# Optimization experiments

Measured on AMD Instinct MI355X. Metric: run time of the kernel, lower is better.

The kernel has to match this reference:

```python
import jax, jax.numpy as jnp
import numpy as np

D2, D1, T1, T2, D3, T3 = 120, 40, 10, 5, 3, 1


def _kaiming_uniform(key, shape):
    # torch kaiming_uniform_ with nonlinearity='relu': bound = sqrt(6/fan_in), fan_in = shape[1]
    bound = np.sqrt(6.0 / shape[1])
    return jax.random.uniform(key, shape, jnp.float32, -bound, bound)


def setup_inputs() -> dict:
    key = jax.random.key(0)
    ks = jax.random.split(key, 6)
    x = jax.random.normal(ks[0], (131072, D1, T1), jnp.float32)
    return {
        "x": x,
        "BL_W1": _kaiming_uniform(ks[1], (D2, D1)),
        "BL_W2": _kaiming_uniform(ks[2], (T1, T2)),
        "BL_B": jnp.zeros((D2, T2), jnp.float32),
        "T_W1": _kaiming_uniform(ks[3], (D3, D2)),
        "T_W": jnp.full((T2, T2), 1.0 / T2, jnp.float32),
        "T_W2": _kaiming_uniform(ks[4], (T2, T3)),
        "T_B": jnp.zeros((D3, T3), jnp.float32),
        "l": jnp.full((1,), 0.5, jnp.float32),
    }


def _max_norm(w):
    # torch max_norm_: if frobenius norm > 10, rescale to norm 10 (done under no_grad)
    n = jnp.linalg.norm(w)
    scale = jnp.where(n > 10.0, 10.0 / (1e-8 + n), 1.0)
    return w * jax.lax.stop_gradient(scale)


def reference(x, BL_W1, BL_W2, BL_B, T_W1, T_W, T_W2, T_B, l):
    # --- weight clamps performed at the top of m_btabl.forward ---
    W1a = _max_norm(BL_W1)
    W2a = _max_norm(BL_W2)
    W1b = _max_norm(T_W1)
    Wb = _max_norm(T_W)
    W2b = _max_norm(T_W2)
    lam = jnp.clip(l[0], 0.0, 1.0)  # l.data clamped to [0,1]

    # BL layer: relu(W1 @ x @ W2 + B); x: [B, D1, T1] -> [B, D2, T2]
    h = jax.nn.relu(jnp.einsum('ed,bdt->bet', W1a, x) @ W2a + BL_B)
    # dropout(0.1) is identity at inference

    # TABL layer (t1 here = T2 = 5)
    X = jnp.einsum('ed,bdt->bet', W1b, h)          # [B, D3, T2]
    eye = jnp.eye(T2, dtype=jnp.float32)
    Wm = Wb - Wb * eye + eye / T2                  # force diagonal to 1/t1
    A = jax.nn.softmax(X @ Wm, axis=-1)            # temporal attention
    X = lam * X + (1.0 - lam) * X * A              # convex combination
    y = X @ W2b + T_B                              # [B, D3, 1]

    y = jnp.squeeze(y)                             # [B, D3]
    return jax.nn.softmax(y, axis=1)
```

## Files before the change

kernel.cpp:

```cpp
#include <hip/hip_runtime.h>
#include <stdint.h>


typedef short bf16x8 __attribute__((ext_vector_type(8)));
typedef float f32x4v __attribute__((ext_vector_type(4)));

#define NTP 256
#define NTM 256

__device__ __forceinline__ unsigned short f2bf(float f) {
    unsigned int u = __float_as_uint(f);
    u += 0x7FFFu + ((u >> 16) & 1u);
    return (unsigned short)(u >> 16);
}

__device__ __forceinline__ float block_reduce_sum(float v, float* red, int tid) {
    #pragma unroll
    for (int off = 32; off > 0; off >>= 1) v += __shfl_xor(v, off, 64);
    if ((tid & 63) == 0) red[tid >> 6] = v;
    __syncthreads();
    float r = red[0] + red[1] + red[2] + red[3];
    __syncthreads();
    return r;
}

__global__ __launch_bounds__(NTP)
void prep_kernel(const float* __restrict__ W1, const float* __restrict__ W2,
                 const float* __restrict__ B,  const float* __restrict__ Tw1,
                 const float* __restrict__ Tw, const float* __restrict__ Tw2,
                 const float* __restrict__ TB, const float* __restrict__ l,
                 float* __restrict__ ws)
{
    __shared__ float red[4];
    const int tid = threadIdx.x;
    float ss;
    ss = 0.f; for (int i = tid; i < 4800; i += NTP) { float w = W1[i];  ss += w*w; }
    const float n1 = sqrtf(block_reduce_sum(ss, red, tid));
    ss = 0.f; for (int i = tid; i < 50;   i += NTP) { float w = W2[i];  ss += w*w; }
    const float n2 = sqrtf(block_reduce_sum(ss, red, tid));
    ss = 0.f; for (int i = tid; i < 360;  i += NTP) { float w = Tw1[i]; ss += w*w; }
    const float n3 = sqrtf(block_reduce_sum(ss, red, tid));
    ss = 0.f; for (int i = tid; i < 25;   i += NTP) { float w = Tw[i];  ss += w*w; }
    const float n4 = sqrtf(block_reduce_sum(ss, red, tid));
    ss = 0.f; for (int i = tid; i < 5;    i += NTP) { float w = Tw2[i]; ss += w*w; }
    const float n5 = sqrtf(block_reduce_sum(ss, red, tid));

    const float s1 = n1 > 10.f ? 10.f/(1e-8f+n1) : 1.f;
    const float s2 = n2 > 10.f ? 10.f/(1e-8f+n2) : 1.f;
    const float s3 = n3 > 10.f ? 10.f/(1e-8f+n3) : 1.f;
    const float s4 = n4 > 10.f ? 10.f/(1e-8f+n4) : 1.f;
    const float s5 = n5 > 10.f ? 10.f/(1e-8f+n5) : 1.f;

    unsigned short* img = (unsigned short*)ws;
    for (int i = tid; i < 129*48; i += NTP) {
        const int e = i / 48, k = i - e*48;
        float v = 0.f;
        if (e < 120) {
            if (k < 40)      v = W1[e*40 + k] * s1;
            else if (k < 45) v = B[e*5 + (k-40)];
        }
        img[i] = f2bf(v);
    }
    for (int i = tid; i < 512; i += NTP) {
        const int e = i >> 2, c = i & 3;
        ws[3096 + i] = (c < 3 && e < 120) ? Tw1[c*120 + e] * s3 : 0.f;
    }
    for (int i = tid; i < 36; i += NTP) {
        float v = 0.f;
        if (i < 25)      { int r = i/5, c = i - r*5; v = (r == c) ? 0.2f : Tw[i]*s4; }
        else if (i < 30) v = Tw2[i-25] * s5;
        else if (i < 33) v = TB[i-30];
        else if (i == 33){ float lv = l[0]; v = fminf(fmaxf(lv, 0.f), 1.f); }
        ws[3608 + i] = v;
    }
    for (int i = tid; i < 50; i += NTP) ws[3644 + i] = W2[i] * s2;
}

__global__ __launch_bounds__(NTM, 4)
void btabl_main(const float* __restrict__ x, const float* __restrict__ ws,
                float* __restrict__ out, int nsamp)
{
    __align__(16) __shared__ unsigned short sW1[129*48];
    __align__(16) __shared__ float          sWp[128*4];
    __align__(16) __shared__ float          sC[36];
    __align__(16) __shared__ unsigned short sZ[320*40 + 32];

    const int tid  = threadIdx.x;
    const int wave = tid >> 6;
    const int lane = tid & 63;

    {
        const float4* src = (const float4*)ws;
        float4* d1 = (float4*)sW1;
        #pragma unroll
        for (int i = 0; i < 4; i++) {
            const int idx = tid + i*NTM;
            if (idx < 774) d1[idx] = src[idx];
        }
        if (tid < 128) ((float4*)sWp)[tid] = src[774 + tid];
        if (tid < 9)   ((float4*)sC)[tid]  = src[902 + tid];
    }
    __syncthreads();

    {
        const float* W2p = ws + 3644;
        #pragma unroll
        for (int r = 0; r < 5; r++) {
            const int job = r*64 + lane;
            const int sl  = job / 20;
            const int r20 = job - sl*20;
            int sG = blockIdx.x*64 + wave*16 + sl;
            sG = sG < nsamp ? sG : (nsamp - 1);
            const float4* xv = (const float4*)(x + (size_t)sG*400 + r20*20);
            float xf[20];
            #pragma unroll
            for (int i = 0; i < 5; i++) {
                const float4 q = xv[i];
                xf[i*4+0] = q.x; xf[i*4+1] = q.y; xf[i*4+2] = q.z; xf[i*4+3] = q.w;
            }
            const int col0 = (wave*16 + sl)*5;
            #pragma unroll
            for (int t = 0; t < 5; t++) {
                float z0 = 0.f, z1 = 0.f;
                #pragma unroll
                for (int k = 0; k < 10; k++) {
                    const float w = W2p[k*5 + t];
                    z0 = fmaf(xf[k],      w, z0);
                    z1 = fmaf(xf[10 + k], w, z1);
                }
                *(unsigned int*)(sZ + (col0 + t)*40 + 2*r20) =
                    (unsigned int)f2bf(z0) | ((unsigned int)f2bf(z1) << 16);
            }
        }
    }

    const int quad = lane >> 4;
    const int m    = lane & 15;
    const int colBase = wave * 80;

    bf16x8 Bf0[5], Bf1[5];
    const bf16x8 z8 = {0,0,0,0,0,0,0,0};
    #pragma unroll
    for (int nt = 0; nt < 5; nt++) {
        const int col = colBase + nt*16 + m;
        Bf0[nt] = *(const bf16x8*)(sZ + col*40 + quad*8);
        const bf16x8 braw = *(const bf16x8*)(sZ + col*40 + (quad == 0 ? 32 : 0));
        bf16x8 v = z8;
        if (quad == 0) v = braw;
        if (quad == 1) {
            const int oh = (nt + m) % 5;
            #pragma unroll
            for (int j = 0; j < 5; j++) v[j] = (oh == j) ? (short)0x3F80 : (short)0;
        }
        Bf1[nt] = v;
    }

    float X3p[5][3];
    #pragma unroll
    for (int nt = 0; nt < 5; nt++)
        #pragma unroll
        for (int j = 0; j < 3; j++) X3p[nt][j] = 0.f;

    const f32x4v zacc = {0.f, 0.f, 0.f, 0.f};
    #pragma unroll
    for (int mt = 0; mt < 8; mt++) {
        const unsigned short* arow = sW1 + (mt*16 + m)*48;
        const bf16x8 A0 = *(const bf16x8*)(arow + quad*8);
        const bf16x8 A1 = *(const bf16x8*)(arow + 32 + quad*8);
        f32x4v wp[4];
        #pragma unroll
        for (int r = 0; r < 4; r++)
            wp[r] = *(const f32x4v*)(sWp + (mt*16 + quad*4 + r)*4);
        #pragma unroll
        for (int nt = 0; nt < 5; nt++) {
            f32x4v acc = __builtin_amdgcn_mfma_f32_16x16x32_bf16(A0, Bf0[nt], zacc, 0, 0, 0);
            acc = __builtin_amdgcn_mfma_f32_16x16x32_bf16(A1, Bf1[nt], acc, 0, 0, 0);
            #pragma unroll
            for (int r = 0; r < 4; r++) {
                const float h = fmaxf(acc[r], 0.f);
                X3p[nt][0] = fmaf(wp[r][0], h, X3p[nt][0]);
                X3p[nt][1] = fmaf(wp[r][1], h, X3p[nt][1]);
                X3p[nt][2] = fmaf(wp[r][2], h, X3p[nt][2]);
            }
        }
    }

    #pragma unroll
    for (int nt = 0; nt < 5; nt++) {
        #pragma unroll
        for (int j = 0; j < 3; j++) {
            float v = X3p[nt][j];
            v += __shfl_xor(v, 16, 64);
            v += __shfl_xor(v, 32, 64);
            X3p[nt][j] = v;
        }
    }
    float* sX3w = (float*)(sZ + wave*3200);
    if (quad == 0) {
        #pragma unroll
        for (int nt = 0; nt < 5; nt++) {
            const int cLoc = nt*16 + m;
            sX3w[cLoc*3 + 0] = X3p[nt][0];
            sX3w[cLoc*3 + 1] = X3p[nt][1];
            sX3w[cLoc*3 + 2] = X3p[nt][2];
        }
    }

    {
        const int sdiv = lane / 3;
        const int j    = lane - sdiv*3;
        const int sLoc = sdiv & 15;
        float X3v[5];
        #pragma unroll
        for (int t = 0; t < 5; t++) X3v[t] = sX3w[(sLoc*5 + t)*3 + j];

        const float lam  = sC[33];
        const float olam = 1.f - lam;
        float S[5];
        #pragma unroll
        for (int t = 0; t < 5; t++) {
            float a = 0.f;
            #pragma unroll
            for (int k = 0; k < 5; k++) a = fmaf(X3v[k], sC[k*5 + t], a);
            S[t] = a;
        }
        float mx = S[0];
        #pragma unroll
        for (int t = 1; t < 5; t++) mx = fmaxf(mx, S[t]);
        float ex[5], se = 0.f;
        #pragma unroll
        for (int t = 0; t < 5; t++) { ex[t] = __expf(S[t] - mx); se += ex[t]; }
        const float inv = 1.f / se;
        float yj = sC[30 + j];
        #pragma unroll
        for (int t = 0; t < 5; t++) {
            const float a  = ex[t] * inv;
            const float xc = X3v[t] * (lam + olam * a);
            yj = fmaf(xc, sC[25 + t], yj);
        }
        const float ya = __shfl(yj, sLoc*3 + 0, 64);
        const float yb = __shfl(yj, sLoc*3 + 1, 64);
        const float yc = __shfl(yj, sLoc*3 + 2, 64);
        const float my = fmaxf(ya, fmaxf(yb, yc));
        const float sse = __expf(ya - my) + __expf(yb - my) + __expf(yc - my);
        const float p = __expf(yj - my) / sse;
        const int sG = blockIdx.x*64 + wave*16 + sLoc;
        if (lane < 48 && sG < nsamp) out[(size_t)sG*3 + j] = p;
    }
}

extern "C" void kernel_launch(void* const* d_in, const int* in_sizes, int n_in,
                              void* d_out, int out_size, void* d_ws, size_t ws_size,
                              hipStream_t stream) {
    const float* x   = (const float*)d_in[0];
    const float* W1  = (const float*)d_in[1];
    const float* W2  = (const float*)d_in[2];
    const float* B   = (const float*)d_in[3];
    const float* Tw1 = (const float*)d_in[4];
    const float* Tw  = (const float*)d_in[5];
    const float* Tw2 = (const float*)d_in[6];
    const float* TB  = (const float*)d_in[7];
    const float* l   = (const float*)d_in[8];
    float* out = (float*)d_out;
    float* ws  = (float*)d_ws;

    hipLaunchKernelGGL(prep_kernel, dim3(1), dim3(NTP), 0, stream,
                       W1, W2, B, Tw1, Tw, Tw2, TB, l, ws);

    const int nsamp = in_sizes[0] / 400;
    const int grid  = (nsamp + 63) / 64;
    hipLaunchKernelGGL(btabl_main, dim3(grid), dim3(NTM), 0, stream,
                       x, ws, out, nsamp);
}
```

Before: 345.9 us.

## Interchange MFMA tile loops to stream B fragments and lower launch-bounds occupancy

The fused MFMA/ReLU/projection stage now loops over column tiles on the outside and row tiles on the inside. Each column tile's B fragments and partial projections are built, reduced across lanes and written to LDS per iteration, so the kernel no longer keeps five B-fragment pairs and a 5x3 accumulator array live at once. The aim is lower register pressure. In exchange, the A fragments and projection weights are reloaded from LDS once per column tile instead of once in total. The launch-bounds minimum is also lowered from 4 to 3 blocks per CU, which gives the compiler more registers per thread but allows fewer resident waves.

```diff
diff --git a/kernel.cpp b/kernel.cpp
--- a/kernel.cpp
+++ b/kernel.cpp
@@ -76,7 +76,7 @@
     for (int i = tid; i < 50; i += NTP) ws[3644 + i] = W2[i] * s2;
 }
 
-__global__ __launch_bounds__(NTM, 4)
+__global__ __launch_bounds__(NTM, 3)
 void btabl_main(const float* __restrict__ x, const float* __restrict__ ws,
                 float* __restrict__ out, int nsamp)
 {
@@ -137,72 +137,48 @@
     const int quad = lane >> 4;
     const int m    = lane & 15;
     const int colBase = wave * 80;
-
-    bf16x8 Bf0[5], Bf1[5];
+    float* sX3w = (float*)(sZ + wave*3200);
+
+    const f32x4v zacc = {0.f, 0.f, 0.f, 0.f};
     const bf16x8 z8 = {0,0,0,0,0,0,0,0};
     #pragma unroll
     for (int nt = 0; nt < 5; nt++) {
         const int col = colBase + nt*16 + m;
-        Bf0[nt] = *(const bf16x8*)(sZ + col*40 + quad*8);
-        const bf16x8 braw = *(const bf16x8*)(sZ + col*40 + (quad == 0 ? 32 : 0));
-        bf16x8 v = z8;
-        if (quad == 0) v = braw;
-        if (quad == 1) {
+        const bf16x8 Bf0 = *(const bf16x8*)(sZ + col*40 + quad*8);
+        bf16x8 Bf1 = z8;
+        if (quad == 0) Bf1 = *(const bf16x8*)(sZ + col*40 + 32);
+        else if (quad == 1) {
             const int oh = (nt + m) % 5;
             #pragma unroll
-            for (int j = 0; j < 5; j++) v[j] = (oh == j) ? (short)0x3F80 : (short)0;
-        }
-        Bf1[nt] = v;
-    }
-
-    float X3p[5][3];
-    #pragma unroll
-    for (int nt = 0; nt < 5; nt++)
-        #pragma unroll
-        for (int j = 0; j < 3; j++) X3p[nt][j] = 0.f;
-
-    const f32x4v zacc = {0.f, 0.f, 0.f, 0.f};
-    #pragma unroll
-    for (int mt = 0; mt < 8; mt++) {
-        const unsigned short* arow = sW1 + (mt*16 + m)*48;
-        const bf16x8 A0 = *(const bf16x8*)(arow + quad*8);
-        const bf16x8 A1 = *(const bf16x8*)(arow + 32 + quad*8);
-        f32x4v wp[4];
-        #pragma unroll
-        for (int r = 0; r < 4; r++)
-            wp[r] = *(const f32x4v*)(sWp + (mt*16 + quad*4 + r)*4);
-        #pragma unroll
-        for (int nt = 0; nt < 5; nt++) {
-            f32x4v acc = __builtin_amdgcn_mfma_f32_16x16x32_bf16(A0, Bf0[nt], zacc, 0, 0, 0);
-            acc = __builtin_amdgcn_mfma_f32_16x16x32_bf16(A1, Bf1[nt], acc, 0, 0, 0);
+            for (int j = 0; j < 5; j++) Bf1[j] = (oh == j) ? (short)0x3F80 : (short)0;
+        }
+
+        float p0 = 0.f, p1 = 0.f, p2 = 0.f;
+        #pragma unroll
+        for (int mt = 0; mt < 8; mt++) {
+            const unsigned short* arow = sW1 + (mt*16 + m)*48;
+            const bf16x8 A0 = *(const bf16x8*)(arow + quad*8);
+            const bf16x8 A1 = *(const bf16x8*)(arow + 32 + quad*8);
+            f32x4v acc = __builtin_amdgcn_mfma_f32_16x16x32_bf16(A0, Bf0, zacc, 0, 0, 0);
+            acc = __builtin_amdgcn_mfma_f32_16x16x32_bf16(A1, Bf1, acc, 0, 0, 0);
             #pragma unroll
             for (int r = 0; r < 4; r++) {
                 const float h = fmaxf(acc[r], 0.f);
-                X3p[nt][0] = fmaf(wp[r][0], h, X3p[nt][0]);
-                X3p[nt][1] = fmaf(wp[r][1], h, X3p[nt][1]);
-                X3p[nt][2] = fmaf(wp[r][2], h, X3p[nt][2]);
+                const f32x4v wp = *(const f32x4v*)(sWp + (mt*16 + quad*4 + r)*4);
+                p0 = fmaf(wp[0], h, p0);
+                p1 = fmaf(wp[1], h, p1);
+                p2 = fmaf(wp[2], h, p2);
             }
         }
-    }
-
-    #pragma unroll
-    for (int nt = 0; nt < 5; nt++) {
-        #pragma unroll
-        for (int j = 0; j < 3; j++) {
-            float v = X3p[nt][j];
-            v += __shfl_xor(v, 16, 64);
-            v += __shfl_xor(v, 32, 64);
-            X3p[nt][j] = v;
-        }
-    }
-    float* sX3w = (float*)(sZ + wave*3200);
-    if (quad == 0) {
-        #pragma unroll
-        for (int nt = 0; nt < 5; nt++) {
+
+        p0 += __shfl_xor(p0, 16, 64); p0 += __shfl_xor(p0, 32, 64);
+        p1 += __shfl_xor(p1, 16, 64); p1 += __shfl_xor(p1, 32, 64);
+        p2 += __shfl_xor(p2, 16, 64); p2 += __shfl_xor(p2, 32, 64);
+        if (quad == 0) {
             const int cLoc = nt*16 + m;
-            sX3w[cLoc*3 + 0] = X3p[nt][0];
-            sX3w[cLoc*3 + 1] = X3p[nt][1];
-            sX3w[cLoc*3 + 2] = X3p[nt][2];
+            sX3w[cLoc*3 + 0] = p0;
+            sX3w[cLoc*3 + 1] = p1;
+            sX3w[cLoc*3 + 2] = p2;
         }
     }
 
```

Result: faster. 330.7 us (-4.4%).
